# Kernel tuning notes

Hardware: AMD Instinct MI355X
Metric: run time of the kernel (lower is better)

The kernel has to match this reference:

```python
import jax, jax.numpy as jnp
import numpy as np

D_MODEL = 768
N_HEAD = 12
D_K = D_MODEL // N_HEAD  # 64, also d_v
B, S = 2, 2048


def setup_inputs() -> dict:
    key = jax.random.key(0)
    ks = jax.random.split(key, 8)
    scale = 1.0 / np.sqrt(D_MODEL)
    return {
        "q": jax.random.normal(ks[0], (B, S, D_MODEL), dtype=jnp.float32),
        "k": jax.random.normal(ks[1], (B, S, D_MODEL), dtype=jnp.float32),
        "v": jax.random.normal(ks[2], (B, S, D_MODEL), dtype=jnp.float32),
        "mask": jax.random.randint(ks[3], (B, 1, S, S), 0, 2, dtype=jnp.int32),
        # per-head projection weights, stacked over heads: [H, d_model, d_k]
        "Wq": jax.random.normal(ks[4], (N_HEAD, D_MODEL, D_K), dtype=jnp.float32) * scale,
        "Wk": jax.random.normal(ks[5], (N_HEAD, D_MODEL, D_K), dtype=jnp.float32) * scale,
        "Wv": jax.random.normal(ks[6], (N_HEAD, D_MODEL, D_K), dtype=jnp.float32) * scale,
        # output projection: [n_head*d_v, d_model]
        "Wo": jax.random.normal(ks[7], (N_HEAD * D_K, D_MODEL), dtype=jnp.float32) * scale,
    }


def reference(q, k, v, mask, Wq, Wk, Wv, Wo):
    # Per-head projections (batched over heads instead of a python loop)
    qh = jnp.einsum("bsd,hdk->bhsk", q, Wq)  # [B,H,S,d_k]
    kh = jnp.einsum("bsd,hdk->bhsk", k, Wk)
    vh = jnp.einsum("bsd,hdk->bhsk", v, Wv)
    # Scaled dot-product attention with full score matrix (faithful to source)
    scores = jnp.einsum("bhsk,bhtk->bhst", qh, kh) / jnp.sqrt(jnp.asarray(D_K, qh.dtype))
    scores = jnp.where(mask == 0, jnp.asarray(-1e9, scores.dtype), scores)
    attn = jax.nn.softmax(scores, axis=-1)  # [B,H,S,S]
    out = jnp.einsum("bhst,bhtk->bhsk", attn, vh)  # [B,H,S,d_k]
    # concat heads (matches torch.cat over head outputs along last dim)
    out = out.transpose(0, 2, 1, 3).reshape(out.shape[0], out.shape[2], -1)  # [B,S,H*d_k]
    return out @ Wo  # [B,S,d_model]
```

## Files before the change

### kernel.cpp

```cpp
#include <hip/hip_runtime.h>
#include <stdint.h>

#define S_LEN 2048
#define NH 12
#define DM 768
#define DK 64
#define NB 2
#define MROWS (NB * S_LEN)

typedef __attribute__((ext_vector_type(8))) short short8;
typedef __attribute__((ext_vector_type(4))) float f32x4;
typedef __attribute__((ext_vector_type(4))) uint32_t u32x4;

__device__ __forceinline__ unsigned short bf16rne(float f) {
    union { float f; uint32_t u; } v; v.f = f;
    return (unsigned short)((v.u + 0x7FFFu + ((v.u >> 16) & 1u)) >> 16);
}

__device__ __forceinline__ uint32_t cvtpk(float lo, float hi) {
    uint32_t r;
    asm("v_cvt_pk_bf16_f32 %0, %1, %2" : "=v"(r) : "v"(lo), "v"(hi));
    return r;
}

__global__ __launch_bounds__(256) void prep_kernel(
        const float* __restrict__ Wq, const float* __restrict__ Wk,
        const float* __restrict__ Wv, const float* __restrict__ Wo,
        const int* __restrict__ mask,
        unsigned short* __restrict__ WqT, unsigned short* __restrict__ WkT,
        unsigned short* __restrict__ WvT, unsigned short* __restrict__ WoT,
        uint32_t* __restrict__ pm) {
    const int bx = blockIdx.x, tid = threadIdx.x;
    if (bx < 576) {
        __shared__ __align__(16) unsigned short L[64 * 72];
        int which, kd0, n0;
        const float* W;
        unsigned short* WT;
        if (bx < 432) {
            which = bx / 144;
            int t2 = bx % 144;
            int h = t2 / 12; kd0 = (t2 % 12) * 64; n0 = h * 64;
            W = (which == 0) ? Wq : (which == 1) ? Wk : Wv;
            WT = (which == 0) ? WqT : (which == 1) ? WkT : WvT;
            const int r = tid >> 2, c0 = (tid & 3) << 4;
            const size_t roff = ((size_t)(h * 768 + kd0 + r)) * 64 + c0;
            float4 f[4];
#pragma unroll
            for (int i = 0; i < 4; ++i) f[i] = *(const float4*)(W + roff + i * 4);
            const float scl = (which == 0) ? 0.18033688011112042f : 1.0f;
#pragma unroll
            for (int i = 0; i < 4; ++i) {
                L[(c0 + i * 4 + 0) * 72 + r] = bf16rne(f[i].x * scl);
                L[(c0 + i * 4 + 1) * 72 + r] = bf16rne(f[i].y * scl);
                L[(c0 + i * 4 + 2) * 72 + r] = bf16rne(f[i].z * scl);
                L[(c0 + i * 4 + 3) * 72 + r] = bf16rne(f[i].w * scl);
            }
        } else {
            int t3 = bx - 432;
            kd0 = (t3 / 12) * 64; n0 = (t3 % 12) * 64;
            WT = WoT;
            const int r = tid >> 2, c0 = (tid & 3) << 4;
            const size_t roff = ((size_t)(kd0 + r)) * 768 + n0 + c0;
            float4 f[4];
#pragma unroll
            for (int i = 0; i < 4; ++i) f[i] = *(const float4*)(Wo + roff + i * 4);
#pragma unroll
            for (int i = 0; i < 4; ++i) {
                L[(c0 + i * 4 + 0) * 72 + r] = bf16rne(f[i].x);
                L[(c0 + i * 4 + 1) * 72 + r] = bf16rne(f[i].y);
                L[(c0 + i * 4 + 2) * 72 + r] = bf16rne(f[i].z);
                L[(c0 + i * 4 + 3) * 72 + r] = bf16rne(f[i].w);
            }
        }
        __syncthreads();
        const int nl = tid >> 2, cc = (tid & 3) << 4;
        short8 v0 = *(const short8*)&L[nl * 72 + cc];
        short8 v1 = *(const short8*)&L[nl * 72 + cc + 8];
        *(short8*)&WT[(size_t)(n0 + nl) * DM + kd0 + cc] = v0;
        *(short8*)&WT[(size_t)(n0 + nl) * DM + kd0 + cc + 8] = v1;
    } else {
        int t = (bx - 576) * 256 + tid;
        const int4* mp = (const int4*)mask;
        int4 a = mp[2 * t], b = mp[2 * t + 1];
        unsigned int by =
            (a.x != 0 ? 1u : 0u)  | (a.y != 0 ? 2u : 0u)  | (a.z != 0 ? 4u : 0u)  | (a.w != 0 ? 8u : 0u) |
            (b.x != 0 ? 16u : 0u) | (b.y != 0 ? 32u : 0u) | (b.z != 0 ? 64u : 0u) | (b.w != 0 ? 128u : 0u);
        ((unsigned char*)pm)[t] = (unsigned char)by;
    }
}

__global__ __launch_bounds__(256) void proj_gemm(
        const float* __restrict__ qf32, const float* __restrict__ kf32,
        const float* __restrict__ vf32,
        const unsigned short* __restrict__ WqT, const unsigned short* __restrict__ WkT,
        const unsigned short* __restrict__ WvT,
        unsigned short* __restrict__ qh, unsigned short* __restrict__ kh,
        unsigned short* __restrict__ vhT) {
    __shared__ __align__(16) unsigned short As[2][128 * 32];
    __shared__ __align__(16) unsigned short Bs[2][128 * 32];
    const int bid = blockIdx.x;
    const int xcd = bid & 7, pos = bid >> 3;
    const int widx = xcd * 72 + pos;
    const int oi = widx / 6, by = widx % 6;
    const int z = oi >> 5, bx = oi & 31;
    const float* A = (z == 0) ? qf32 : (z == 1) ? kf32 : vf32;
    const unsigned short* BT = (z == 0) ? WqT : (z == 1) ? WkT : WvT;
    const int tid = threadIdx.x;
    const int lane = tid & 63, wid = tid >> 6;
    const int ww = wid & 1, wh = wid >> 1;
    const int quad = lane >> 4, l16 = lane & 15;
    const int lr = lane >> 2, lc = (lane & 3) * 8;
    typedef __attribute__((address_space(1))) const unsigned int* gp1;
    typedef __attribute__((address_space(3))) unsigned int* lp3;
    const float* Ag0 = A + (size_t)(bx * 128 + wid * 32 + lr) * DM + lc;
    const float* Ag1 = Ag0 + 16 * DM;
    const unsigned short* Bg = BT + (size_t)(by * 128 + wid * 32 + lr) * DM + lc;
    const int wb = wid * 1024;

    f32x4 acc[4][4] = {};
    {
        float4 x0 = *(const float4*)(Ag0), x1 = *(const float4*)(Ag0 + 4);
        float4 y0 = *(const float4*)(Ag1), y1 = *(const float4*)(Ag1 + 4);
        __builtin_amdgcn_global_load_lds((gp1)(const void*)(Bg),           (lp3)(void*)&Bs[0][wb],       16, 0, 0);
        __builtin_amdgcn_global_load_lds((gp1)(const void*)(Bg + 16 * DM), (lp3)(void*)&Bs[0][wb + 512], 16, 0, 0);
        u32x4 ua, ub;
        ua[0] = cvtpk(x0.x, x0.y); ua[1] = cvtpk(x0.z, x0.w);
        ua[2] = cvtpk(x1.x, x1.y); ua[3] = cvtpk(x1.z, x1.w);
        ub[0] = cvtpk(y0.x, y0.y); ub[1] = cvtpk(y0.z, y0.w);
        ub[2] = cvtpk(y1.x, y1.y); ub[3] = cvtpk(y1.z, y1.w);
        *(u32x4*)&As[0][wb + lr * 32 + lc] = ua;
        *(u32x4*)&As[0][wb + (16 + lr) * 32 + lc] = ub;
    }
    __syncthreads();
    int cur = 0;
    for (int kt = 0; kt < DM; kt += 32) {
        const bool more = (kt + 32) < DM;
        float4 nx0, nx1, ny0, ny1;
        if (more) {
            nx0 = *(const float4*)(Ag0 + kt + 32); nx1 = *(const float4*)(Ag0 + kt + 36);
            ny0 = *(const float4*)(Ag1 + kt + 32); ny1 = *(const float4*)(Ag1 + kt + 36);
            __builtin_amdgcn_global_load_lds((gp1)(const void*)(Bg + kt + 32),            (lp3)(void*)&Bs[cur ^ 1][wb],       16, 0, 0);
            __builtin_amdgcn_global_load_lds((gp1)(const void*)(Bg + kt + 32 + 16 * DM),  (lp3)(void*)&Bs[cur ^ 1][wb + 512], 16, 0, 0);
        }
        short8 af[4], bf[4];
#pragma unroll
        for (int i = 0; i < 4; ++i) af[i] = *(const short8*)&As[cur][(wh * 64 + i * 16 + l16) * 32 + quad * 8];
#pragma unroll
        for (int j = 0; j < 4; ++j) bf[j] = *(const short8*)&Bs[cur][(ww * 64 + j * 16 + l16) * 32 + quad * 8];
#pragma unroll
        for (int i = 0; i < 4; ++i)
#pragma unroll
            for (int j = 0; j < 4; ++j)
                acc[i][j] = __builtin_amdgcn_mfma_f32_16x16x32_bf16(af[i], bf[j], acc[i][j], 0, 0, 0);
        if (more) {
            u32x4 ua, ub;
            ua[0] = cvtpk(nx0.x, nx0.y); ua[1] = cvtpk(nx0.z, nx0.w);
            ua[2] = cvtpk(nx1.x, nx1.y); ua[3] = cvtpk(nx1.z, nx1.w);
            ub[0] = cvtpk(ny0.x, ny0.y); ub[1] = cvtpk(ny0.z, ny0.w);
            ub[2] = cvtpk(ny1.x, ny1.y); ub[3] = cvtpk(ny1.z, ny1.w);
            *(u32x4*)&As[cur ^ 1][wb + lr * 32 + lc] = ua;
            *(u32x4*)&As[cur ^ 1][wb + (16 + lr) * 32 + lc] = ub;
        }
        __syncthreads();
        cur ^= 1;
    }

    const int row0 = bx * 128 + wh * 64;
    const int col0 = by * 128 + ww * 64;
    if (z < 2) {
        unsigned short* C = z ? kh : qh;
#pragma unroll
        for (int i = 0; i < 4; ++i)
#pragma unroll
            for (int j = 0; j < 4; ++j)
#pragma unroll
                for (int r = 0; r < 4; ++r)
                    C[(size_t)(row0 + i * 16 + quad * 4 + r) * DM + col0 + j * 16 + l16] = bf16rne(acc[i][j][r]);
    } else {
#pragma unroll
        for (int i = 0; i < 4; ++i)
#pragma unroll
            for (int j = 0; j < 4; ++j) {
                int row = row0 + i * 16 + quad * 4;
                int col = col0 + j * 16 + l16;
                int bb = row >> 11, s = row & 2047;
                int hh = col >> 6, d = col & 63;
                int g = (s >> 2) & 15;
                int pg = (g & 8) | ((g & 3) << 1) | ((g & 4) >> 2);
                int sp = (s & ~63) | (pg << 2) | (s & 3);
                uint32_t lo = (uint32_t)bf16rne(acc[i][j][0]) | ((uint32_t)bf16rne(acc[i][j][1]) << 16);
                uint32_t hi = (uint32_t)bf16rne(acc[i][j][2]) | ((uint32_t)bf16rne(acc[i][j][3]) << 16);
                uint2 o = make_uint2(lo, hi);
                *(uint2*)&vhT[(size_t)((bb * NH + hh) * DK + d) * S_LEN + sp] = o;
            }
    }
}

__global__ __launch_bounds__(256) void attn_kernel(
        const unsigned short* __restrict__ qh, const unsigned short* __restrict__ kh,
        const unsigned short* __restrict__ vhT, const uint32_t* __restrict__ pm,
        unsigned short* __restrict__ pob, float* __restrict__ lsb) {
    const int bid = blockIdx.x;
    const int xcd = bid & 7, pos = bid >> 3;
    const int wkr = xcd * 192 + pos;
    const int qt = wkr & 15;
    const int hz = wkr >> 4;
    const int h = hz % 12;
    const int z = hz / 12;
    const int b = z >> 2, ks = z & 3;
    const int tid = threadIdx.x, w = tid >> 6, lane = tid & 63;
    const int quad = lane >> 4, l16 = lane & 15;
    __shared__ __align__(16) unsigned short SMEM[2 * 2 * 64 * 64];

    const int qrow0 = qt * 128 + w * 32;
    short8 qf[2][2];
#pragma unroll
    for (int mi = 0; mi < 2; ++mi) {
        const size_t qbase = (size_t)(b * S_LEN + qrow0 + mi * 16 + l16) * DM + h * DK;
        qf[mi][0] = *(const short8*)&qh[qbase + quad * 8];
        qf[mi][1] = *(const short8*)&qh[qbase + 32 + quad * 8];
    }
    short8 of = {};
    if (l16 == 0) {
#pragma unroll
        for (int j = 0; j < 8; ++j) of[j] = (short)0x3F80;
    }

    f32x4 out_t[2][4] = {};
    f32x4 outl[2] = {};

    const int srow = tid >> 2, scol = (tid & 3) << 4;
    const int ssw = (srow & 7) << 3;
    const int sc0 = srow * 64 + (scol ^ ssw);
    const int sc1 = srow * 64 + ((scol + 8) ^ ssw);
    const unsigned short* Kg = kh + (size_t)b * S_LEN * DM + h * DK;
    const unsigned short* Vg = vhT + (size_t)((b * NH + h) * DK) * S_LEN;
    const int kt0 = ks * (S_LEN / 4);
    const int NT = (S_LEN / 4) / 64;

    {
        short8 a0 = *(const short8*)&Kg[(size_t)(kt0 + srow) * DM + scol];
        short8 a1 = *(const short8*)&Kg[(size_t)(kt0 + srow) * DM + scol + 8];
        short8 a2 = *(const short8*)&Vg[(size_t)srow * S_LEN + kt0 + scol];
        short8 a3 = *(const short8*)&Vg[(size_t)srow * S_LEN + kt0 + scol + 8];
        *(short8*)&SMEM[sc0] = a0;
        *(short8*)&SMEM[sc1] = a1;
        *(short8*)&SMEM[4096 + sc0] = a2;
        *(short8*)&SMEM[4096 + sc1] = a3;
    }
    __syncthreads();

    int cur = 0;
    for (int t = 0; t < NT; ++t) {
        const int kt = kt0 + t * 64;
        const bool more = (t + 1 < NT);
        short8 kr0, kr1, vr0, vr1;
        if (more) {
            const int kn = kt + 64;
            kr0 = *(const short8*)&Kg[(size_t)(kn + srow) * DM + scol];
            kr1 = *(const short8*)&Kg[(size_t)(kn + srow) * DM + scol + 8];
            vr0 = *(const short8*)&Vg[(size_t)srow * S_LEN + kn + scol];
            vr1 = *(const short8*)&Vg[(size_t)srow * S_LEN + kn + scol + 8];
        }
        uint2 mw[2];
#pragma unroll
        for (int mi = 0; mi < 2; ++mi)
            mw[mi] = *(const uint2*)&pm[(size_t)(b * S_LEN + qrow0 + mi * 16 + l16) * 64 + (kt >> 5)];

        const unsigned short* Ks = SMEM + cur * 8192;
        const unsigned short* Vs = Ks + 4096;

        u32x4 pf32[2][2];
#pragma unroll
        for (int cb = 0; cb < 4; ++cb) {
            const int krw = cb * 16 + l16, ksw = (krw & 7) << 3;
            short8 kf0 = *(const short8*)&Ks[krw * 64 + ((quad * 8) ^ ksw)];
            short8 kf1 = *(const short8*)&Ks[krw * 64 + ((32 + quad * 8) ^ ksw)];
#pragma unroll
            for (int mi = 0; mi < 2; ++mi) {
                f32x4 zz = {0.f, 0.f, 0.f, 0.f};
                zz = __builtin_amdgcn_mfma_f32_16x16x32_bf16(kf0, qf[mi][0], zz, 0, 0, 0);
                zz = __builtin_amdgcn_mfma_f32_16x16x32_bf16(kf1, qf[mi][1], zz, 0, 0, 0);
                uint32_t mword = (cb & 2) ? mw[mi].y : mw[mi].x;
                float e[4];
#pragma unroll
                for (int r = 0; r < 4; ++r) {
                    float ev = __builtin_amdgcn_exp2f(zz[r]);
                    int32_t mneg = __builtin_amdgcn_sbfe((int32_t)mword, ((cb & 1) << 4) + quad * 4 + r, 1);
                    e[r] = __uint_as_float(__float_as_uint(ev) & (uint32_t)mneg);
                }
                pf32[mi][cb >> 1][(cb & 1) * 2 + 0] = cvtpk(e[0], e[1]);
                pf32[mi][cb >> 1][(cb & 1) * 2 + 1] = cvtpk(e[2], e[3]);
            }
        }
        short8 pf[2][2];
#pragma unroll
        for (int mi = 0; mi < 2; ++mi) {
            pf[mi][0] = __builtin_bit_cast(short8, pf32[mi][0]);
            pf[mi][1] = __builtin_bit_cast(short8, pf32[mi][1]);
        }

        __builtin_amdgcn_s_setprio(1);
#pragma unroll
        for (int c2 = 0; c2 < 4; ++c2) {
            const int vrw = c2 * 16 + l16, vsw = (vrw & 7) << 3;
            short8 vf0 = *(const short8*)&Vs[vrw * 64 + ((quad * 8) ^ vsw)];
            short8 vf1 = *(const short8*)&Vs[vrw * 64 + ((32 + quad * 8) ^ vsw)];
#pragma unroll
            for (int mi = 0; mi < 2; ++mi) {
                out_t[mi][c2] = __builtin_amdgcn_mfma_f32_16x16x32_bf16(vf0, pf[mi][0], out_t[mi][c2], 0, 0, 0);
                out_t[mi][c2] = __builtin_amdgcn_mfma_f32_16x16x32_bf16(vf1, pf[mi][1], out_t[mi][c2], 0, 0, 0);
            }
        }
#pragma unroll
        for (int mi = 0; mi < 2; ++mi) {
            outl[mi] = __builtin_amdgcn_mfma_f32_16x16x32_bf16(of, pf[mi][0], outl[mi], 0, 0, 0);
            outl[mi] = __builtin_amdgcn_mfma_f32_16x16x32_bf16(of, pf[mi][1], outl[mi], 0, 0, 0);
        }
        __builtin_amdgcn_s_setprio(0);

        if (more) {
            unsigned short* Kn = SMEM + (cur ^ 1) * 8192;
            *(short8*)&Kn[sc0] = kr0;
            *(short8*)&Kn[sc1] = kr1;
            *(short8*)&Kn[4096 + sc0] = vr0;
            *(short8*)&Kn[4096 + sc1] = vr1;
            __syncthreads();
            cur ^= 1;
        }
    }

    const int pz = z;
    if (quad == 0) {
#pragma unroll
        for (int mi = 0; mi < 2; ++mi)
            lsb[((size_t)pz * NH + h) * S_LEN + qrow0 + mi * 16 + l16] = outl[mi][0];
    }

    __syncthreads();
    unsigned short* Os = SMEM + w * 2048;
#pragma unroll
    for (int mi = 0; mi < 2; ++mi) {
        const int orow = mi * 16 + l16, osw = (orow & 7) << 3;
#pragma unroll
        for (int c2 = 0; c2 < 4; ++c2) {
            uint2 pw2;
            pw2.x = cvtpk(out_t[mi][c2][0], out_t[mi][c2][1]);
            pw2.y = cvtpk(out_t[mi][c2][2], out_t[mi][c2][3]);
            *(uint2*)&Os[orow * 64 + ((c2 * 16 + quad * 4) ^ osw)] = pw2;
        }
    }
    const int ql = lane >> 1, hf = lane & 1;
    const int qsw = (ql & 7) << 3;
    const int qg = qrow0 + ql;
    const size_t orowg = ((size_t)pz * S_LEN + qg) * DM + h * DK + hf * 32;
#pragma unroll
    for (int k2 = 0; k2 < 4; ++k2)
        *(short8*)&pob[orowg + k2 * 8] = *(const short8*)&Os[ql * 64 + ((hf * 32 + k2 * 8) ^ qsw)];
}

__global__ __launch_bounds__(256) void out_gemm(
        const unsigned short* __restrict__ pob, const float* __restrict__ lsb,
        const unsigned short* __restrict__ WoT, float* __restrict__ C) {
    __shared__ __align__(16) unsigned short As[2][128 * 32];
    __shared__ __align__(16) unsigned short Bs[2][128 * 32];
    const int bid = blockIdx.x;
    const int xcd = bid & 7, pos = bid >> 3;
    const int widx = xcd * 24 + pos;
    const int bx = widx / 6, by = widx % 6;
    const int tid = threadIdx.x;
    const int lane = tid & 63, wid = tid >> 6;
    const int ww = wid & 1, wh = wid >> 1;
    const int quad = lane >> 4, l16 = lane & 15;
    const int lr = lane >> 2, lc = (lane & 3) * 8;
    typedef __attribute__((address_space(1))) const unsigned int* gp1;
    typedef __attribute__((address_space(3))) unsigned int* lp3;
    const int ra0 = bx * 128 + wid * 32 + lr;
    const int ra1 = ra0 + 16;
    const int bb = bx >> 4;
    const unsigned short* Bg = WoT + (size_t)(by * 128 + wid * 32 + lr) * DM + lc;
    const int wb = wid * 1024;
    size_t oa0[4], oa1[4];
    int ol0[4], ol1[4];
#pragma unroll
    for (int ksp = 0; ksp < 4; ++ksp) {
        int pz = bb * 4 + ksp;
        oa0[ksp] = ((size_t)pz * S_LEN + (ra0 & 2047)) * DM + lc;
        oa1[ksp] = ((size_t)pz * S_LEN + (ra1 & 2047)) * DM + lc;
        ol0[ksp] = (pz * NH) * S_LEN + (ra0 & 2047);
        ol1[ksp] = (pz * NH) * S_LEN + (ra1 & 2047);
    }
    f32x4 acc[4][4] = {};

    short8 p0[4], p1[4];
    float s0[4], s1[4];
    {
#pragma unroll
        for (int ksp = 0; ksp < 4; ++ksp) { s0[ksp] = lsb[ol0[ksp]]; s1[ksp] = lsb[ol1[ksp]]; }
#pragma unroll
        for (int ksp = 0; ksp < 4; ++ksp) { p0[ksp] = *(const short8*)&pob[oa0[ksp]]; p1[ksp] = *(const short8*)&pob[oa1[ksp]]; }
        __builtin_amdgcn_global_load_lds((gp1)(const void*)(Bg),           (lp3)(void*)&Bs[0][wb],       16, 0, 0);
        __builtin_amdgcn_global_load_lds((gp1)(const void*)(Bg + 16 * DM), (lp3)(void*)&Bs[0][wb + 512], 16, 0, 0);
        float l0 = s0[0] + s0[1] + s0[2] + s0[3];
        float l1 = s1[0] + s1[1] + s1[2] + s1[3];
        float rl0 = 1.f / fmaxf(l0, 1e-37f);
        float rl1 = 1.f / fmaxf(l1, 1e-37f);
        u32x4 ua, ub;
#pragma unroll
        for (int e = 0; e < 4; ++e) {
            float f0lo = 0.f, f0hi = 0.f, f1lo = 0.f, f1hi = 0.f;
#pragma unroll
            for (int ksp = 0; ksp < 4; ++ksp) {
                uint32_t w0 = ((const u32x4&)p0[ksp])[e];
                uint32_t w1 = ((const u32x4&)p1[ksp])[e];
                f0lo += __uint_as_float(w0 << 16);
                f0hi += __uint_as_float(w0 & 0xFFFF0000u);
                f1lo += __uint_as_float(w1 << 16);
                f1hi += __uint_as_float(w1 & 0xFFFF0000u);
            }
            ua[e] = cvtpk(f0lo * rl0, f0hi * rl0);
            ub[e] = cvtpk(f1lo * rl1, f1hi * rl1);
        }
        *(u32x4*)&As[0][wb + lr * 32 + lc] = ua;
        *(u32x4*)&As[0][wb + (16 + lr) * 32 + lc] = ub;
    }
    __syncthreads();
    int cur = 0;
    for (int kt = 0; kt < DM; kt += 32) {
        const bool more = (kt + 32) < DM;
        if (more) {
            const int hh = (kt + 32) >> 6;
#pragma unroll
            for (int ksp = 0; ksp < 4; ++ksp) { s0[ksp] = lsb[ol0[ksp] + hh * S_LEN]; s1[ksp] = lsb[ol1[ksp] + hh * S_LEN]; }
#pragma unroll
            for (int ksp = 0; ksp < 4; ++ksp) { p0[ksp] = *(const short8*)&pob[oa0[ksp] + kt + 32]; p1[ksp] = *(const short8*)&pob[oa1[ksp] + kt + 32]; }
            __builtin_amdgcn_global_load_lds((gp1)(const void*)(Bg + kt + 32),           (lp3)(void*)&Bs[cur ^ 1][wb],       16, 0, 0);
            __builtin_amdgcn_global_load_lds((gp1)(const void*)(Bg + kt + 32 + 16 * DM), (lp3)(void*)&Bs[cur ^ 1][wb + 512], 16, 0, 0);
        }
        short8 af[4], bf[4];
#pragma unroll
        for (int i = 0; i < 4; ++i) af[i] = *(const short8*)&As[cur][(wh * 64 + i * 16 + l16) * 32 + quad * 8];
#pragma unroll
        for (int j = 0; j < 4; ++j) bf[j] = *(const short8*)&Bs[cur][(ww * 64 + j * 16 + l16) * 32 + quad * 8];
#pragma unroll
        for (int i = 0; i < 4; ++i)
#pragma unroll
            for (int j = 0; j < 4; ++j)
                acc[i][j] = __builtin_amdgcn_mfma_f32_16x16x32_bf16(af[i], bf[j], acc[i][j], 0, 0, 0);
        if (more) {
            float l0 = s0[0] + s0[1] + s0[2] + s0[3];
            float l1 = s1[0] + s1[1] + s1[2] + s1[3];
            float rl0 = 1.f / fmaxf(l0, 1e-37f);
            float rl1 = 1.f / fmaxf(l1, 1e-37f);
            u32x4 ua, ub;
#pragma unroll
            for (int e = 0; e < 4; ++e) {
                float f0lo = 0.f, f0hi = 0.f, f1lo = 0.f, f1hi = 0.f;
#pragma unroll
                for (int ksp = 0; ksp < 4; ++ksp) {
                    uint32_t w0 = ((const u32x4&)p0[ksp])[e];
                    uint32_t w1 = ((const u32x4&)p1[ksp])[e];
                    f0lo += __uint_as_float(w0 << 16);
                    f0hi += __uint_as_float(w0 & 0xFFFF0000u);
                    f1lo += __uint_as_float(w1 << 16);
                    f1hi += __uint_as_float(w1 & 0xFFFF0000u);
                }
                ua[e] = cvtpk(f0lo * rl0, f0hi * rl0);
                ub[e] = cvtpk(f1lo * rl1, f1hi * rl1);
            }
            *(u32x4*)&As[cur ^ 1][wb + lr * 32 + lc] = ua;
            *(u32x4*)&As[cur ^ 1][wb + (16 + lr) * 32 + lc] = ub;
        }
        __syncthreads();
        cur ^= 1;
    }
    const int row0 = bx * 128 + wh * 64;
    const int col0 = by * 128 + ww * 64;
#pragma unroll
    for (int i = 0; i < 4; ++i)
#pragma unroll
        for (int j = 0; j < 4; ++j)
#pragma unroll
            for (int r = 0; r < 4; ++r)
                C[(size_t)(row0 + i * 16 + quad * 4 + r) * DM + col0 + j * 16 + l16] = acc[i][j][r];
}

extern "C" void kernel_launch(void* const* d_in, const int* in_sizes, int n_in,
                              void* d_out, int out_size, void* d_ws, size_t ws_size,
                              hipStream_t stream) {
    const float* q = (const float*)d_in[0];
    const float* k = (const float*)d_in[1];
    const float* v = (const float*)d_in[2];
    const int* mask = (const int*)d_in[3];
    const float* Wq = (const float*)d_in[4];
    const float* Wk = (const float*)d_in[5];
    const float* Wv = (const float*)d_in[6];
    const float* Wo = (const float*)d_in[7];
    float* out = (float*)d_out;

    char* ws = (char*)d_ws;
    size_t off = 0;
    auto alloc = [&](size_t bytes) {
        void* p = ws + off;
        off += (bytes + 255) & ~(size_t)255;
        return p;
    };
    const size_t MAT = (size_t)MROWS * DM * 2;
    const size_t WMAT = (size_t)DM * DM * 2;
    unsigned short* WoT = (unsigned short*)alloc(WMAT);
    unsigned short* qh  = (unsigned short*)alloc(MAT);
    unsigned short* kh  = (unsigned short*)alloc(MAT);
    unsigned short* vhT = (unsigned short*)alloc(MAT);
    uint32_t* pmask     = (uint32_t*)alloc((size_t)NB * S_LEN * 64 * 4);
    float* lsb          = (float*)alloc((size_t)8 * NH * S_LEN * 4);
    unsigned short* WqT = (unsigned short*)alloc(WMAT);
    unsigned short* WkT = (unsigned short*)alloc(WMAT);
    unsigned short* WvT = (unsigned short*)alloc(WMAT);
    unsigned short* pob = WqT;
    (void)alloc((size_t)8 * S_LEN * DM * 2 - 3 * WMAT);

    prep_kernel<<<dim3(576 + 4096), 256, 0, stream>>>(Wq, Wk, Wv, Wo, mask,
                                                      WqT, WkT, WvT, WoT, pmask);
    proj_gemm<<<dim3(576), 256, 0, stream>>>(q, k, v, WqT, WkT, WvT, qh, kh, vhT);
    attn_kernel<<<dim3(1536), 256, 0, stream>>>(qh, kh, vhT, pmask, pob, lsb);
    out_gemm<<<dim3(192), 256, 0, stream>>>(pob, lsb, WoT, out);
}
```

Measured before the change: 231.2 us.

## Split split-K merge into its own kernel and shrink GEMM tiles for more blocks

The projection GEMM tile goes from 128x128 to 128x64, doubling the grid to 1152 blocks. The split-K softmax merge that out_gemm used to do inline is moved into a separate merge_kernel, which writes normalized bf16 attention output into the reused qh buffer. out_gemm then becomes a plain bf16 64x64-tile GEMM over 768 blocks. The goal is better CU occupancy on the small grids (192 out_gemm blocks before) and a simpler out_gemm inner loop. The cost is an extra launch, an extra round trip of the merged activations through memory, and smaller tiles with less reuse.

Measured after the change: 232.9 us. No clear change (+0.7%).

```diff
diff --git a/kernel.cpp b/kernel.cpp
--- a/kernel.cpp
+++ b/kernel.cpp
@@ -33,14 +33,13 @@
     const int bx = blockIdx.x, tid = threadIdx.x;
     if (bx < 576) {
         __shared__ __align__(16) unsigned short L[64 * 72];
-        int which, kd0, n0;
-        const float* W;
+        int kd0, n0;
         unsigned short* WT;
         if (bx < 432) {
-            which = bx / 144;
+            int which = bx / 144;
             int t2 = bx % 144;
             int h = t2 / 12; kd0 = (t2 % 12) * 64; n0 = h * 64;
-            W = (which == 0) ? Wq : (which == 1) ? Wk : Wv;
+            const float* W = (which == 0) ? Wq : (which == 1) ? Wk : Wv;
             WT = (which == 0) ? WqT : (which == 1) ? WkT : WvT;
             const int r = tid >> 2, c0 = (tid & 3) << 4;
             const size_t roff = ((size_t)(h * 768 + kd0 + r)) * 64 + c0;
@@ -97,11 +96,11 @@
         unsigned short* __restrict__ qh, unsigned short* __restrict__ kh,
         unsigned short* __restrict__ vhT) {
     __shared__ __align__(16) unsigned short As[2][128 * 32];
-    __shared__ __align__(16) unsigned short Bs[2][128 * 32];
+    __shared__ __align__(16) unsigned short Bs[2][64 * 32];
     const int bid = blockIdx.x;
     const int xcd = bid & 7, pos = bid >> 3;
-    const int widx = xcd * 72 + pos;
-    const int oi = widx / 6, by = widx % 6;
+    const int widx = xcd * 144 + pos;
+    const int oi = widx / 12, by = widx % 12;
     const int z = oi >> 5, bx = oi & 31;
     const float* A = (z == 0) ? qf32 : (z == 1) ? kf32 : vf32;
     const unsigned short* BT = (z == 0) ? WqT : (z == 1) ? WkT : WvT;
@@ -112,67 +111,66 @@
     const int lr = lane >> 2, lc = (lane & 3) * 8;
     typedef __attribute__((address_space(1))) const unsigned int* gp1;
     typedef __attribute__((address_space(3))) unsigned int* lp3;
-    const float* Ag0 = A + (size_t)(bx * 128 + wid * 32 + lr) * DM + lc;
-    const float* Ag1 = Ag0 + 16 * DM;
-    const unsigned short* Bg = BT + (size_t)(by * 128 + wid * 32 + lr) * DM + lc;
-    const int wb = wid * 1024;
-
-    f32x4 acc[4][4] = {};
+    const int ar = tid >> 1, ahk = (tid & 1) * 16;
+    const float* Ag = A + (size_t)(bx * 128 + ar) * DM + ahk;
+    const int aoff = ar * 32 + ahk;
+    const unsigned short* Bg = BT + (size_t)(by * 64 + wid * 16 + lr) * DM + lc;
+    const int boff = wid * 16 * 32;
+
+    f32x4 acc[4][2] = {};
     {
-        float4 x0 = *(const float4*)(Ag0), x1 = *(const float4*)(Ag0 + 4);
-        float4 y0 = *(const float4*)(Ag1), y1 = *(const float4*)(Ag1 + 4);
-        __builtin_amdgcn_global_load_lds((gp1)(const void*)(Bg),           (lp3)(void*)&Bs[0][wb],       16, 0, 0);
-        __builtin_amdgcn_global_load_lds((gp1)(const void*)(Bg + 16 * DM), (lp3)(void*)&Bs[0][wb + 512], 16, 0, 0);
-        u32x4 ua, ub;
-        ua[0] = cvtpk(x0.x, x0.y); ua[1] = cvtpk(x0.z, x0.w);
-        ua[2] = cvtpk(x1.x, x1.y); ua[3] = cvtpk(x1.z, x1.w);
-        ub[0] = cvtpk(y0.x, y0.y); ub[1] = cvtpk(y0.z, y0.w);
-        ub[2] = cvtpk(y1.x, y1.y); ub[3] = cvtpk(y1.z, y1.w);
-        *(u32x4*)&As[0][wb + lr * 32 + lc] = ua;
-        *(u32x4*)&As[0][wb + (16 + lr) * 32 + lc] = ub;
+        float4 x0 = *(const float4*)(Ag);     float4 x1 = *(const float4*)(Ag + 4);
+        float4 x2 = *(const float4*)(Ag + 8); float4 x3 = *(const float4*)(Ag + 12);
+        __builtin_amdgcn_global_load_lds((gp1)(const void*)Bg, (lp3)(void*)&Bs[0][boff], 16, 0, 0);
+        u32x4 u0, u1;
+        u0[0] = cvtpk(x0.x, x0.y); u0[1] = cvtpk(x0.z, x0.w);
+        u0[2] = cvtpk(x1.x, x1.y); u0[3] = cvtpk(x1.z, x1.w);
+        u1[0] = cvtpk(x2.x, x2.y); u1[1] = cvtpk(x2.z, x2.w);
+        u1[2] = cvtpk(x3.x, x3.y); u1[3] = cvtpk(x3.z, x3.w);
+        *(u32x4*)&As[0][aoff] = u0;
+        *(u32x4*)&As[0][aoff + 8] = u1;
     }
     __syncthreads();
     int cur = 0;
     for (int kt = 0; kt < DM; kt += 32) {
         const bool more = (kt + 32) < DM;
-        float4 nx0, nx1, ny0, ny1;
-        if (more) {
-            nx0 = *(const float4*)(Ag0 + kt + 32); nx1 = *(const float4*)(Ag0 + kt + 36);
-            ny0 = *(const float4*)(Ag1 + kt + 32); ny1 = *(const float4*)(Ag1 + kt + 36);
-            __builtin_amdgcn_global_load_lds((gp1)(const void*)(Bg + kt + 32),            (lp3)(void*)&Bs[cur ^ 1][wb],       16, 0, 0);
-            __builtin_amdgcn_global_load_lds((gp1)(const void*)(Bg + kt + 32 + 16 * DM),  (lp3)(void*)&Bs[cur ^ 1][wb + 512], 16, 0, 0);
-        }
-        short8 af[4], bf[4];
+        float4 x0, x1, x2, x3;
+        if (more) {
+            x0 = *(const float4*)(Ag + kt + 32); x1 = *(const float4*)(Ag + kt + 36);
+            x2 = *(const float4*)(Ag + kt + 40); x3 = *(const float4*)(Ag + kt + 44);
+            __builtin_amdgcn_global_load_lds((gp1)(const void*)(Bg + kt + 32), (lp3)(void*)&Bs[cur ^ 1][boff], 16, 0, 0);
+        }
+        short8 af[4], bf[2];
 #pragma unroll
         for (int i = 0; i < 4; ++i) af[i] = *(const short8*)&As[cur][(wh * 64 + i * 16 + l16) * 32 + quad * 8];
 #pragma unroll
-        for (int j = 0; j < 4; ++j) bf[j] = *(const short8*)&Bs[cur][(ww * 64 + j * 16 + l16) * 32 + quad * 8];
+        for (int j = 0; j < 2; ++j) bf[j] = *(const short8*)&Bs[cur][(ww * 32 + j * 16 + l16) * 32 + quad * 8];
 #pragma unroll
         for (int i = 0; i < 4; ++i)
 #pragma unroll
-            for (int j = 0; j < 4; ++j)
+            for (int j = 0; j < 2; ++j)
                 acc[i][j] = __builtin_amdgcn_mfma_f32_16x16x32_bf16(af[i], bf[j], acc[i][j], 0, 0, 0);
         if (more) {
-            u32x4 ua, ub;
-            ua[0] = cvtpk(nx0.x, nx0.y); ua[1] = cvtpk(nx0.z, nx0.w);
-            ua[2] = cvtpk(nx1.x, nx1.y); ua[3] = cvtpk(nx1.z, nx1.w);
-            ub[0] = cvtpk(ny0.x, ny0.y); ub[1] = cvtpk(ny0.z, ny0.w);
-            ub[2] = cvtpk(ny1.x, ny1.y); ub[3] = cvtpk(ny1.z, ny1.w);
-            *(u32x4*)&As[cur ^ 1][wb + lr * 32 + lc] = ua;
-            *(u32x4*)&As[cur ^ 1][wb + (16 + lr) * 32 + lc] = ub;
-        }
-        __syncthreads();
-        cur ^= 1;
+            u32x4 u0, u1;
+            u0[0] = cvtpk(x0.x, x0.y); u0[1] = cvtpk(x0.z, x0.w);
+            u0[2] = cvtpk(x1.x, x1.y); u0[3] = cvtpk(x1.z, x1.w);
+            u1[0] = cvtpk(x2.x, x2.y); u1[1] = cvtpk(x2.z, x2.w);
+            u1[2] = cvtpk(x3.x, x3.y); u1[3] = cvtpk(x3.z, x3.w);
+            *(u32x4*)&As[cur ^ 1][aoff] = u0;
+            *(u32x4*)&As[cur ^ 1][aoff + 8] = u1;
+            __syncthreads();
+            cur ^= 1;
+        }
     }
 
     const int row0 = bx * 128 + wh * 64;
-    const int col0 = by * 128 + ww * 64;
+    const int col0 = by * 64 + ww * 32;
     if (z < 2) {
         unsigned short* C = z ? kh : qh;
 #pragma unroll
         for (int i = 0; i < 4; ++i)
 #pragma unroll
-            for (int j = 0; j < 4; ++j)
+            for (int j = 0; j < 2; ++j)
 #pragma unroll
                 for (int r = 0; r < 4; ++r)
                     C[(size_t)(row0 + i * 16 + quad * 4 + r) * DM + col0 + j * 16 + l16] = bf16rne(acc[i][j][r]);
@@ -180,7 +178,7 @@
 #pragma unroll
         for (int i = 0; i < 4; ++i)
 #pragma unroll
-            for (int j = 0; j < 4; ++j) {
+            for (int j = 0; j < 2; ++j) {
                 int row = row0 + i * 16 + quad * 4;
                 int col = col0 + j * 16 + l16;
                 int bb = row >> 11, s = row & 2047;
@@ -359,15 +357,41 @@
         *(short8*)&pob[orowg + k2 * 8] = *(const short8*)&Os[ql * 64 + ((hf * 32 + k2 * 8) ^ qsw)];
 }
 
+__global__ __launch_bounds__(256) void merge_kernel(const unsigned short* __restrict__ pob,
+                                                    const float* __restrict__ lsb,
+                                                    unsigned short* __restrict__ ao) {
+    int t = blockIdx.x * 256 + threadIdx.x;
+    int sg = t / 192;
+    int c = (t - sg * 192) * 4;
+    int b = sg >> 11, s = sg & 2047, h = c >> 6;
+    float l = 0.f;
+#pragma unroll
+    for (int ksp = 0; ksp < 4; ++ksp)
+        l += lsb[((size_t)(b * 4 + ksp) * NH + h) * S_LEN + s];
+    float rl = 1.f / fmaxf(l, 1e-37f);
+    float f0 = 0.f, f1 = 0.f, f2 = 0.f, f3 = 0.f;
+#pragma unroll
+    for (int ksp = 0; ksp < 4; ++ksp) {
+        uint2 a = *(const uint2*)&pob[((size_t)((b * 4 + ksp) * S_LEN) + s) * DM + c];
+        f0 += __uint_as_float(a.x << 16);
+        f1 += __uint_as_float(a.x & 0xFFFF0000u);
+        f2 += __uint_as_float(a.y << 16);
+        f3 += __uint_as_float(a.y & 0xFFFF0000u);
+    }
+    uint32_t lo = cvtpk(f0 * rl, f1 * rl);
+    uint32_t hi = cvtpk(f2 * rl, f3 * rl);
+    *(uint2*)&ao[(size_t)sg * DM + c] = make_uint2(lo, hi);
+}
+
 __global__ __launch_bounds__(256) void out_gemm(
-        const unsigned short* __restrict__ pob, const float* __restrict__ lsb,
-        const unsigned short* __restrict__ WoT, float* __restrict__ C) {
-    __shared__ __align__(16) unsigned short As[2][128 * 32];
-    __shared__ __align__(16) unsigned short Bs[2][128 * 32];
+        const unsigned short* __restrict__ ao, const unsigned short* __restrict__ WoT,
+        float* __restrict__ C) {
+    __shared__ __align__(16) unsigned short As[2][64 * 32];
+    __shared__ __align__(16) unsigned short Bs[2][64 * 32];
     const int bid = blockIdx.x;
     const int xcd = bid & 7, pos = bid >> 3;
-    const int widx = xcd * 24 + pos;
-    const int bx = widx / 6, by = widx % 6;
+    const int widx = xcd * 96 + pos;
+    const int bx = widx / 12, by = widx % 12;
     const int tid = threadIdx.x;
     const int lane = tid & 63, wid = tid >> 6;
     const int ww = wid & 1, wh = wid >> 1;
@@ -375,111 +399,41 @@
     const int lr = lane >> 2, lc = (lane & 3) * 8;
     typedef __attribute__((address_space(1))) const unsigned int* gp1;
     typedef __attribute__((address_space(3))) unsigned int* lp3;
-    const int ra0 = bx * 128 + wid * 32 + lr;
-    const int ra1 = ra0 + 16;
-    const int bb = bx >> 4;
-    const unsigned short* Bg = WoT + (size_t)(by * 128 + wid * 32 + lr) * DM + lc;
-    const int wb = wid * 1024;
-    size_t oa0[4], oa1[4];
-    int ol0[4], ol1[4];
-#pragma unroll
-    for (int ksp = 0; ksp < 4; ++ksp) {
-        int pz = bb * 4 + ksp;
-        oa0[ksp] = ((size_t)pz * S_LEN + (ra0 & 2047)) * DM + lc;
-        oa1[ksp] = ((size_t)pz * S_LEN + (ra1 & 2047)) * DM + lc;
-        ol0[ksp] = (pz * NH) * S_LEN + (ra0 & 2047);
-        ol1[ksp] = (pz * NH) * S_LEN + (ra1 & 2047);
-    }
-    f32x4 acc[4][4] = {};
-
-    short8 p0[4], p1[4];
-    float s0[4], s1[4];
-    {
-#pragma unroll
-        for (int ksp = 0; ksp < 4; ++ksp) { s0[ksp] = lsb[ol0[ksp]]; s1[ksp] = lsb[ol1[ksp]]; }
-#pragma unroll
-        for (int ksp = 0; ksp < 4; ++ksp) { p0[ksp] = *(const short8*)&pob[oa0[ksp]]; p1[ksp] = *(const short8*)&pob[oa1[ksp]]; }
-        __builtin_amdgcn_global_load_lds((gp1)(const void*)(Bg),           (lp3)(void*)&Bs[0][wb],       16, 0, 0);
-        __builtin_amdgcn_global_load_lds((gp1)(const void*)(Bg + 16 * DM), (lp3)(void*)&Bs[0][wb + 512], 16, 0, 0);
-        float l0 = s0[0] + s0[1] + s0[2] + s0[3];
-        float l1 = s1[0] + s1[1] + s1[2] + s1[3];
-        float rl0 = 1.f / fmaxf(l0, 1e-37f);
-        float rl1 = 1.f / fmaxf(l1, 1e-37f);
-        u32x4 ua, ub;
-#pragma unroll
-        for (int e = 0; e < 4; ++e) {
-            float f0lo = 0.f, f0hi = 0.f, f1lo = 0.f, f1hi = 0.f;
-#pragma unroll
-            for (int ksp = 0; ksp < 4; ++ksp) {
-                uint32_t w0 = ((const u32x4&)p0[ksp])[e];
-                uint32_t w1 = ((const u32x4&)p1[ksp])[e];
-                f0lo += __uint_as_float(w0 << 16);
-                f0hi += __uint_as_float(w0 & 0xFFFF0000u);
-                f1lo += __uint_as_float(w1 << 16);
-                f1hi += __uint_as_float(w1 & 0xFFFF0000u);
-            }
-            ua[e] = cvtpk(f0lo * rl0, f0hi * rl0);
-            ub[e] = cvtpk(f1lo * rl1, f1hi * rl1);
-        }
-        *(u32x4*)&As[0][wb + lr * 32 + lc] = ua;
-        *(u32x4*)&As[0][wb + (16 + lr) * 32 + lc] = ub;
-    }
+    const unsigned short* Ag = ao  + (size_t)(bx * 64 + wid * 16 + lr) * DM + lc;
+    const unsigned short* Bg = WoT + (size_t)(by * 64 + wid * 16 + lr) * DM + lc;
+    const int soff = wid * 16 * 32;
+    f32x4 acc[2][2] = {};
+    __builtin_amdgcn_global_load_lds((gp1)(const void*)Ag, (lp3)(void*)&As[0][soff], 16, 0, 0);
+    __builtin_amdgcn_global_load_lds((gp1)(const void*)Bg, (lp3)(void*)&Bs[0][soff], 16, 0, 0);
     __syncthreads();
     int cur = 0;
     for (int kt = 0; kt < DM; kt += 32) {
         const bool more = (kt + 32) < DM;
         if (more) {
-            const int hh = (kt + 32) >> 6;
-#pragma unroll
-            for (int ksp = 0; ksp < 4; ++ksp) { s0[ksp] = lsb[ol0[ksp] + hh * S_LEN]; s1[ksp] = lsb[ol1[ksp] + hh * S_LEN]; }
-#pragma unroll
-            for (int ksp = 0; ksp < 4; ++ksp) { p0[ksp] = *(const short8*)&pob[oa0[ksp] + kt + 32]; p1[ksp] = *(const short8*)&pob[oa1[ksp] + kt + 32]; }
-            __builtin_amdgcn_global_load_lds((gp1)(const void*)(Bg + kt + 32),           (lp3)(void*)&Bs[cur ^ 1][wb],       16, 0, 0);
-            __builtin_amdgcn_global_load_lds((gp1)(const void*)(Bg + kt + 32 + 16 * DM), (lp3)(void*)&Bs[cur ^ 1][wb + 512], 16, 0, 0);
-        }
-        short8 af[4], bf[4];
-#pragma unroll
-        for (int i = 0; i < 4; ++i) af[i] = *(const short8*)&As[cur][(wh * 64 + i * 16 + l16) * 32 + quad * 8];
-#pragma unroll
-        for (int j = 0; j < 4; ++j) bf[j] = *(const short8*)&Bs[cur][(ww * 64 + j * 16 + l16) * 32 + quad * 8];
-#pragma unroll
-        for (int i = 0; i < 4; ++i)
-#pragma unroll
-            for (int j = 0; j < 4; ++j)
+            __builtin_amdgcn_global_load_lds((gp1)(const void*)(Ag + kt + 32), (lp3)(void*)&As[cur ^ 1][soff], 16, 0, 0);
+            __builtin_amdgcn_global_load_lds((gp1)(const void*)(Bg + kt + 32), (lp3)(void*)&Bs[cur ^ 1][soff], 16, 0, 0);
+        }
+        short8 af[2], bf[2];
+#pragma unroll
+        for (int i = 0; i < 2; ++i) af[i] = *(const short8*)&As[cur][(wh * 32 + i * 16 + l16) * 32 + quad * 8];
+#pragma unroll
+        for (int j = 0; j < 2; ++j) bf[j] = *(const short8*)&Bs[cur][(ww * 32 + j * 16 + l16) * 32 + quad * 8];
+#pragma unroll
+        for (int i = 0; i < 2; ++i)
+#pragma unroll
+            for (int j = 0; j < 2; ++j)
                 acc[i][j] = __builtin_amdgcn_mfma_f32_16x16x32_bf16(af[i], bf[j], acc[i][j], 0, 0, 0);
         if (more) {
-            float l0 = s0[0] + s0[1] + s0[2] + s0[3];
-            float l1 = s1[0] + s1[1] + s1[2] + s1[3];
-            float rl0 = 1.f / fmaxf(l0, 1e-37f);
-            float rl1 = 1.f / fmaxf(l1, 1e-37f);
-            u32x4 ua, ub;
-#pragma unroll
-            for (int e = 0; e < 4; ++e) {
-                float f0lo = 0.f, f0hi = 0.f, f1lo = 0.f, f1hi = 0.f;
-#pragma unroll
-                for (int ksp = 0; ksp < 4; ++ksp) {
-                    uint32_t w0 = ((const u32x4&)p0[ksp])[e];
-                    uint32_t w1 = ((const u32x4&)p1[ksp])[e];
-                    f0lo += __uint_as_float(w0 << 16);
-                    f0hi += __uint_as_float(w0 & 0xFFFF0000u);
-                    f1lo += __uint_as_float(w1 << 16);
-                    f1hi += __uint_as_float(w1 & 0xFFFF0000u);
-                }
-                ua[e] = cvtpk(f0lo * rl0, f0hi * rl0);
-                ub[e] = cvtpk(f1lo * rl1, f1hi * rl1);
-            }
-            *(u32x4*)&As[cur ^ 1][wb + lr * 32 + lc] = ua;
-            *(u32x4*)&As[cur ^ 1][wb + (16 + lr) * 32 + lc] = ub;
-        }
-        __syncthreads();
-        cur ^= 1;
-    }
-    const int row0 = bx * 128 + wh * 64;
-    const int col0 = by * 128 + ww * 64;
-#pragma unroll
-    for (int i = 0; i < 4; ++i)
-#pragma unroll
-        for (int j = 0; j < 4; ++j)
+            __syncthreads();
+            cur ^= 1;
+        }
+    }
+    const int row0 = bx * 64 + wh * 32;
+    const int col0 = by * 64 + ww * 32;
+#pragma unroll
+    for (int i = 0; i < 2; ++i)
+#pragma unroll
+        for (int j = 0; j < 2; ++j)
 #pragma unroll
             for (int r = 0; r < 4; ++r)
                 C[(size_t)(row0 + i * 16 + quad * 4 + r) * DM + col0 + j * 16 + l16] = acc[i][j][r];
@@ -518,10 +472,12 @@
     unsigned short* WvT = (unsigned short*)alloc(WMAT);
     unsigned short* pob = WqT;
     (void)alloc((size_t)8 * S_LEN * DM * 2 - 3 * WMAT);
+    unsigned short* ao = qh;
 
     prep_kernel<<<dim3(576 + 4096), 256, 0, stream>>>(Wq, Wk, Wv, Wo, mask,
                                                       WqT, WkT, WvT, WoT, pmask);
-    proj_gemm<<<dim3(576), 256, 0, stream>>>(q, k, v, WqT, WkT, WvT, qh, kh, vhT);
+    proj_gemm<<<dim3(1152), 256, 0, stream>>>(q, k, v, WqT, WkT, WvT, qh, kh, vhT);
     attn_kernel<<<dim3(1536), 256, 0, stream>>>(qh, kh, vhT, pmask, pob, lsb);
-    out_gemm<<<dim3(192), 256, 0, stream>>>(pob, lsb, WoT, out);
-}
+    merge_kernel<<<dim3(3072), 256, 0, stream>>>(pob, lsb, ao);
+    out_gemm<<<dim3(768), 256, 0, stream>>>(ao, WoT, out);
+}
```
